# Optimization experiments

Hardware: AMD Instinct MI355X
Metric: run time of the kernel (lower is better)

## Reference

```python
import jax, jax.numpy as jnp
import numpy as np

D_MODEL = 256
N_HEADS = 8
HEAD_DIM = D_MODEL // N_HEADS


def setup_inputs() -> dict:
    key = jax.random.key(0)
    ks = jax.random.split(key, 10)
    B, L, D = 2, 2048, D_MODEL
    s = 1.0 / np.sqrt(D)
    inp = {
        "x": jax.random.normal(ks[0], (B, L, D), dtype=jnp.float32),
        "Wq": jax.random.normal(ks[1], (D, D), dtype=jnp.float32) * s,
        "bq": jnp.zeros((D,), jnp.float32),
        "Wk": jax.random.normal(ks[2], (D, D), dtype=jnp.float32) * s,
        "bk": jnp.zeros((D,), jnp.float32),
        "Wv": jax.random.normal(ks[3], (D, D), dtype=jnp.float32) * s,
        "bv": jnp.zeros((D,), jnp.float32),
        "u": jax.random.normal(ks[4], (N_HEADS, 1, 1), dtype=jnp.float32) * 0.1,
        "Wo": jax.random.normal(ks[5], (D, D), dtype=jnp.float32) * s,
        "bo": jnp.zeros((D,), jnp.float32),
    }
    return inp


def reference(x, Wq, bq, Wk, bk, Wv, bv, u, Wo, bo):
    B, L, D = x.shape
    H, hd = N_HEADS, HEAD_DIM

    def proj(W, b):  # torch Linear: x @ W.T + b -> [B,H,L,hd]
        return (x @ W.T + b).reshape(B, L, H, hd).transpose(0, 2, 1, 3)

    Q, K, V = proj(Wq, bq), proj(Wk, bk), proj(Wv, bv)

    scores = jnp.einsum("bhqd,bhkd->bhqk", Q, K) / np.sqrt(hd)
    attn_series = jax.nn.softmax(scores, axis=-1)  # [B,H,L,L]

    pos = jnp.arange(L, dtype=jnp.float32)
    dist = jnp.abs(pos[None, :] - pos[:, None])  # [L,L]
    # prior per head: exp(-d^2 / (2*(u^2+1e-6))), normalized over last dim
    prior = jnp.exp(-(dist[None] ** 2) / (2.0 * (u ** 2 + 1e-6)))  # [H,L,L]
    prior = prior / (prior.sum(axis=-1, keepdims=True) + 1e-6)

    discrepancy = jnp.abs(attn_series - prior[None]).mean(axis=(1, 2))  # [B,L]

    out = jnp.einsum("bhqk,bhkd->bhqd", attn_series, V)
    out = out.transpose(0, 2, 1, 3).reshape(B, L, D)
    out = out @ Wo.T + bo
    return out, discrepancy
```

## Files before the change

### kernel.cpp

```cpp
#include <hip/hip_runtime.h>
#include <hip/hip_bf16.h>
#include <math.h>

#define LSEQ 2048
#define DMODEL 256
#define NH 8
#define HD 32

typedef __attribute__((ext_vector_type(8))) short bf16x8;
typedef __attribute__((ext_vector_type(4))) float f32x4;

#define MFMA __builtin_amdgcn_mfma_f32_16x16x32_bf16

__device__ __forceinline__ short f2bf(float x) {
  __hip_bfloat16 h = __float2bfloat16(x);
  return __builtin_bit_cast(short, h);
}
__device__ __forceinline__ float bf2f(short s) {
  __hip_bfloat16 h = __builtin_bit_cast(__hip_bfloat16, s);
  return __bfloat162float(h);
}
__device__ __forceinline__ short bftrunc(float x) {
  return (short)(__builtin_bit_cast(unsigned int, x) >> 16);
}
__device__ __forceinline__ float fexp2(float x) {
#if __has_builtin(__builtin_amdgcn_exp2f)
  return __builtin_amdgcn_exp2f(x);
#else
  return __expf(x * 0.6931471805599453f);
#endif
}
__device__ __forceinline__ float flog2(float x) {
#if __has_builtin(__builtin_amdgcn_logf)
  return __builtin_amdgcn_logf(x);
#else
  return __logf(x) * 1.4426950408889634f;
#endif
}

__global__ __launch_bounds__(256) void aux_kernel(
    const float* __restrict__ Wq, const float* __restrict__ Wk,
    const float* __restrict__ Wv, const float* __restrict__ Wo,
    const float* __restrict__ u,
    short* __restrict__ Wh,
    short* __restrict__ Woh, short* __restrict__ Wol,
    float* __restrict__ Eb, float* __restrict__ Zb,
    float* __restrict__ disc)
{
  __shared__ float Cs[LSEQ];
  __shared__ float part[256];
  const int tid = threadIdx.x;
  if (blockIdx.x < 256) {
    const int i4 = (blockIdx.x * 256 + tid) * 4;
    if (i4 < 196608) {
      int row = i4 >> 8, col = i4 & 255;
      const float* W = (row < 256) ? Wq : (row < 512) ? Wk : Wv;
      float4 v = *(const float4*)(W + (row & 255) * 256 + col);
      *(short4*)(Wh + i4) = make_short4(f2bf(v.x), f2bf(v.y), f2bf(v.z), f2bf(v.w));
    } else {
      int j = i4 - 196608;
      float4 v = *(const float4*)(Wo + j);
      short h0 = f2bf(v.x), h1 = f2bf(v.y), h2 = f2bf(v.z), h3 = f2bf(v.w);
      *(short4*)(Woh + j) = make_short4(h0, h1, h2, h3);
      *(short4*)(Wol + j) = make_short4(bftrunc(v.x - bf2f(h0)), bftrunc(v.y - bf2f(h1)),
                                        bftrunc(v.z - bf2f(h2)), bftrunc(v.w - bf2f(h3)));
    }
    return;
  }
  const int h = blockIdx.x - 256;
  const float uu = u[h];
  const float den = 2.0f * (uu * uu + 1e-6f);
  float e[8]; float run = 0.f;
  const int base = tid * 8;
#pragma unroll
  for (int j = 0; j < 8; ++j) {
    float d = (float)(base + j);
    e[j] = __expf(-(d * d) / den);
    run += e[j];
  }
  part[tid] = run;
  __syncthreads();
  for (int off = 1; off < 256; off <<= 1) {
    float v = (tid >= off) ? part[tid - off] : 0.f;
    __syncthreads();
    part[tid] += v;
    __syncthreads();
  }
  float c = part[tid] - run;
#pragma unroll
  for (int j = 0; j < 8; ++j) {
    c += e[j];
    Cs[base + j] = c;
    Eb[h * LSEQ + base + j] = e[j];
  }
  __syncthreads();
  const float E0 = Cs[0];
  for (int i = tid; i < LSEQ; i += 256) {
    float s = Cs[i] + Cs[LSEQ - 1 - i] - E0;
    Zb[h * LSEQ + i] = 1.0f / (s + 1e-6f);
  }
  for (int i = tid; i < 512; i += 256) disc[h * 512 + i] = 0.f;
}

__global__ __launch_bounds__(256) void qkv_gemm(
    const float* __restrict__ x,
    const short* __restrict__ Bh,
    const float* __restrict__ bq, const float* __restrict__ bk,
    const float* __restrict__ bv,
    short* __restrict__ Qf, short* __restrict__ Kf, short* __restrict__ Vf)
{
  const int tid = threadIdx.x, w = tid >> 6, lane = tid & 63;
  const int l15 = lane & 15, q4 = lane >> 4;
  const int m0 = blockIdx.x * 64, n0 = blockIdx.y * 64;
  const int mrow = m0 + w * 16 + l15;
  f32x4 acc[4] = {{0,0,0,0},{0,0,0,0},{0,0,0,0},{0,0,0,0}};
  for (int k0 = 0; k0 < 256; k0 += 32) {
    const float* xp = &x[(size_t)mrow * 256 + k0 + q4 * 8];
    float4 a = *(const float4*)xp;
    float4 c = *(const float4*)(xp + 4);
    bf16x8 ah;
    ah[0] = f2bf(a.x); ah[1] = f2bf(a.y); ah[2] = f2bf(a.z); ah[3] = f2bf(a.w);
    ah[4] = f2bf(c.x); ah[5] = f2bf(c.y); ah[6] = f2bf(c.z); ah[7] = f2bf(c.w);
#pragma unroll
    for (int nt = 0; nt < 4; ++nt) {
      const size_t bi = (size_t)(n0 + nt * 16 + l15) * 256 + k0 + q4 * 8;
      bf16x8 bh = *(const bf16x8*)&Bh[bi];
      acc[nt] = MFMA(ah, bh, acc[nt], 0, 0, 0);
    }
  }
  const int type = n0 >> 8;
  const int n0l = n0 & 255;
  const float* bias = (type == 0) ? bq : (type == 1) ? bk : bv;
  const float qls = 0.25503489f;
#pragma unroll
  for (int nt = 0; nt < 4; ++nt) {
    const int col = n0l + nt * 16 + l15;
    const float bvv = bias[col];
    const int hh = col >> 5, dloc = col & 31;
#pragma unroll
    for (int r = 0; r < 4; ++r) {
      const int m = m0 + w * 16 + q4 * 4 + r;
      float v = acc[nt][r] + bvv;
      const int bb = m >> 11, mm = m & 2047, rr = mm & 15;
      if (type == 2) {
        const int kt128 = mm >> 7, low7 = mm & 127;
        const int wv = (low7 >> 4) & 3, ph = low7 >> 6;
        const int c = ph * 16 + rr;
        const size_t idx =
          ((((((size_t)bb * 8 + hh) * 16 + kt128) * 4 + wv) * 2 + (dloc >> 4)) * 64
           + (c >> 3) * 16 + (dloc & 15)) * 8 + (c & 7);
        Vf[idx] = f2bf(v);
      } else if (type == 0) {
        const int qblk = mm >> 5, rg = (mm >> 4) & 1;
        const size_t idx =
          (((((size_t)bb * 8 + hh) * 64 + qblk) * 2 + rg) * 64
           + (dloc >> 3) * 16 + rr) * 8 + (dloc & 7);
        Qf[idx] = f2bf(v * qls);
      } else {
        const int g = mm >> 4;
        const size_t idx =
          ((((size_t)bb * 8 + hh) * 128 + g) * 64
           + (dloc >> 3) * 16 + rr) * 8 + (dloc & 7);
        Kf[idx] = f2bf(v);
      }
    }
  }
}

__global__ __launch_bounds__(256) void out_gemm(
    const short* __restrict__ Ah, const short* __restrict__ Al,
    const short* __restrict__ Bh, const short* __restrict__ Bl,
    const float* __restrict__ bias, float* __restrict__ C)
{
  const int tid = threadIdx.x, w = tid >> 6, lane = tid & 63;
  const int l15 = lane & 15, q4 = lane >> 4;
  const int m0 = blockIdx.x * 64, n0 = blockIdx.y * 64;
  const int mrow = m0 + w * 16 + l15;
  f32x4 acc[4] = {{0,0,0,0},{0,0,0,0},{0,0,0,0},{0,0,0,0}};
  for (int k0 = 0; k0 < 256; k0 += 32) {
    bf16x8 ah = *(const bf16x8*)&Ah[(size_t)mrow * 256 + k0 + q4 * 8];
    bf16x8 al = *(const bf16x8*)&Al[(size_t)mrow * 256 + k0 + q4 * 8];
#pragma unroll
    for (int nt = 0; nt < 4; ++nt) {
      const size_t bi = (size_t)(n0 + nt * 16 + l15) * 256 + k0 + q4 * 8;
      bf16x8 bh = *(const bf16x8*)&Bh[bi];
      bf16x8 bl = *(const bf16x8*)&Bl[bi];
      acc[nt] = MFMA(ah, bh, acc[nt], 0, 0, 0);
      acc[nt] = MFMA(al, bh, acc[nt], 0, 0, 0);
      acc[nt] = MFMA(ah, bl, acc[nt], 0, 0, 0);
    }
  }
#pragma unroll
  for (int nt = 0; nt < 4; ++nt) {
    const int col = n0 + nt * 16 + l15;
    const float bvv = bias[col];
#pragma unroll
    for (int r = 0; r < 4; ++r) {
      const int m = m0 + w * 16 + q4 * 4 + r;
      C[(size_t)m * 256 + col] = acc[nt][r] + bvv;
    }
  }
}

__global__ __launch_bounds__(256, 4) void attn_kernel(
    const short* __restrict__ Qf, const short* __restrict__ Kf,
    const short* __restrict__ Vf,
    const float* __restrict__ Eb, const float* __restrict__ Zb,
    short* __restrict__ Ohb, short* __restrict__ Olb,
    float* __restrict__ disc)
{
  __shared__ short Pt[4][32][40];
  __shared__ float Elds[192];
  __shared__ float dcol[LSEQ];
  __shared__ float lpart[4][32];
  __shared__ float izlds[32];

  const int tid = threadIdx.x, w = tid >> 6, lane = tid & 63;
  const int l15 = lane & 15, q4 = lane >> 4;
  const int flat = blockIdx.x + 64 * (blockIdx.y + 8 * blockIdx.z);
  const int slot = flat >> 3;
  const int g = (flat & 7) | ((slot >> 6) << 3);
  const int h = g & 7, b = g >> 3;
  const int q0 = (slot & 63) * 32;
  const int bh = b * NH + h;

  for (int i = tid; i < LSEQ; i += 256) dcol[i] = 0.f;
  if (tid < 192) Elds[tid] = Eb[h * LSEQ + tid];
  if (tid < 32)  izlds[tid] = Zb[h * LSEQ + q0 + tid];

  const bf16x8* Qf8 = (const bf16x8*)Qf;
  const bf16x8* Kf8 = (const bf16x8*)Kf;
  const bf16x8* Vf8 = (const bf16x8*)Vf;

  bf16x8 qh[2];
#pragma unroll
  for (int rg = 0; rg < 2; ++rg)
    qh[rg] = Qf8[((((size_t)bh * 64 + (q0 >> 5)) * 2 + rg)) * 64 + lane];
  __syncthreads();

  const size_t kfb = (size_t)bh * 128;
  const size_t vfb = (size_t)bh * 16;

  float lac[2][4] = {{0,0,0,0},{0,0,0,0}};
#pragma unroll 2
  for (int kt = 0; kt < LSEQ; kt += 128) {
    bf16x8 k0 = Kf8[(kfb + (kt >> 4) + w) * 64 + lane];
    bf16x8 k1 = Kf8[(kfb + (kt >> 4) + 4 + w) * 64 + lane];
#pragma unroll
    for (int rg = 0; rg < 2; ++rg) {
      f32x4 s0 = {0.f, 0.f, 0.f, 0.f};
      s0 = MFMA(qh[rg], k0, s0, 0, 0, 0);
      f32x4 s1 = {0.f, 0.f, 0.f, 0.f};
      s1 = MFMA(qh[rg], k1, s1, 0, 0, 0);
#pragma unroll
      for (int r = 0; r < 4; ++r) lac[rg][r] += fexp2(s0[r]) + fexp2(s1[r]);
    }
  }
#pragma unroll
  for (int rg = 0; rg < 2; ++rg)
#pragma unroll
    for (int r = 0; r < 4; ++r) {
      float v = lac[rg][r];
      v += __shfl_xor(v, 1); v += __shfl_xor(v, 2);
      v += __shfl_xor(v, 4); v += __shfl_xor(v, 8);
      lac[rg][r] = v;
    }
  if (l15 == 0) {
#pragma unroll
    for (int rg = 0; rg < 2; ++rg)
#pragma unroll
      for (int r = 0; r < 4; ++r) lpart[w][rg * 16 + q4 * 4 + r] = lac[rg][r];
  }
  __syncthreads();
  f32x4 sinit[2];
#pragma unroll
  for (int rg = 0; rg < 2; ++rg)
#pragma unroll
    for (int r = 0; r < 4; ++r) {
      const int qi = rg * 16 + q4 * 4 + r;
      sinit[rg][r] = -flog2(lpart[0][qi] + lpart[1][qi] + lpart[2][qi] + lpart[3][qi]);
    }

  f32x4 oacc[2][2] = {{{0,0,0,0},{0,0,0,0}},{{0,0,0,0},{0,0,0,0}}};
#pragma unroll 2
  for (int kt = 0; kt < LSEQ; kt += 128) {
    bf16x8 kh0 = Kf8[(kfb + (kt >> 4) + w) * 64 + lane];
    bf16x8 kh1 = Kf8[(kfb + (kt >> 4) + 4 + w) * 64 + lane];
    bf16x8 vb0 = Vf8[(((vfb + (kt >> 7)) * 4 + w) * 2 + 0) * 64 + lane];
    bf16x8 vb1 = Vf8[(((vfb + (kt >> 7)) * 4 + w) * 2 + 1) * 64 + lane];
#pragma unroll
    for (int ph = 0; ph < 2; ++ph) {
      bf16x8 kbh = ph ? kh1 : kh0;
      const int c0 = kt + ph * 64 + w * 16;
      const int kg = c0 + l15;
      const int dd = c0 - q0;
      const bool near = (dd >= -96) && (dd <= 96);
      float dsum = 0.f;
#pragma unroll
      for (int rg = 0; rg < 2; ++rg) {
        f32x4 s = sinit[rg];
        s = MFMA(qh[rg], kbh, s, 0, 0, 0);
#pragma unroll
        for (int r = 0; r < 4; ++r) {
          float p = fexp2(s[r]);
          Pt[w][rg * 16 + q4 * 4 + r][ph * 16 + l15] = bftrunc(p);
          if (near) {
            int qrow = q0 + rg * 16 + q4 * 4 + r;
            int dist = (qrow >= kg) ? (qrow - kg) : (kg - qrow);
            dsum += fabsf(p - Elds[dist] * izlds[rg * 16 + q4 * 4 + r]);
          } else {
            dsum += p;
          }
        }
      }
      dsum += __shfl_xor(dsum, 16);
      dsum += __shfl_xor(dsum, 32);
      if (q4 == 0) atomicAdd(&dcol[kg], dsum);
    }
#pragma unroll
    for (int rg = 0; rg < 2; ++rg) {
      bf16x8 pa = *(const bf16x8*)&Pt[w][rg * 16 + l15][q4 * 8];
      oacc[rg][0] = MFMA(pa, vb0, oacc[rg][0], 0, 0, 0);
      oacc[rg][1] = MFMA(pa, vb1, oacc[rg][1], 0, 0, 0);
    }
  }

  __syncthreads();
  float* Ored = (float*)&Pt[0][0][0];
#pragma unroll
  for (int dt = 0; dt < 2; ++dt) {
#pragma unroll
    for (int rg = 0; rg < 2; ++rg)
#pragma unroll
      for (int r = 0; r < 4; ++r)
        Ored[(w * 32 + rg * 16 + q4 * 4 + r) * 17 + l15] = oacc[rg][dt][r];
    __syncthreads();
    for (int t = tid; t < 512; t += 256) {
      const int q = t >> 4, d = t & 15;
      float v = Ored[(q) * 17 + d] + Ored[(32 + q) * 17 + d] +
                Ored[(64 + q) * 17 + d] + Ored[(96 + q) * 17 + d];
      const size_t oo = ((size_t)b * LSEQ + q0 + q) * DMODEL + h * HD + dt * 16 + d;
      short hi = f2bf(v);
      Ohb[oo] = hi;
      Olb[oo] = bftrunc(v - bf2f(hi));
    }
    __syncthreads();
  }
  const float sc = 1.0f / (float)(NH * LSEQ);
  for (int i = tid; i < LSEQ; i += 256)
    atomicAdd(&disc[(size_t)b * LSEQ + i], dcol[i] * sc);
}

extern "C" void kernel_launch(void* const* d_in, const int* in_sizes, int n_in,
                              void* d_out, int out_size, void* d_ws, size_t ws_size,
                              hipStream_t stream)
{
  const float* x  = (const float*)d_in[0];
  const float* Wq = (const float*)d_in[1];
  const float* bq = (const float*)d_in[2];
  const float* Wk = (const float*)d_in[3];
  const float* bk = (const float*)d_in[4];
  const float* Wv = (const float*)d_in[5];
  const float* bv = (const float*)d_in[6];
  const float* u  = (const float*)d_in[7];
  const float* Wo = (const float*)d_in[8];
  const float* bo = (const float*)d_in[9];

  float* out  = (float*)d_out;
  float* disc = out + (size_t)2 * LSEQ * DMODEL;

  char* w8 = (char*)d_ws;
  const size_t MB = 1u << 20;
  short* Qfb = (short*)(w8);
  short* Kfb = (short*)(w8 + 2 * MB);
  short* Vfb = (short*)(w8 + 4 * MB);
  short* Ohb = (short*)(w8 + 6 * MB);
  short* Olb = (short*)(w8 + 8 * MB);
  short* Wh  = (short*)(w8 + 10 * MB);
  short* Woh = (short*)(w8 + 10 * MB + 393216);
  short* Wol = (short*)(w8 + 10 * MB + 524288);
  float* Eb  = (float*)(w8 + 11 * MB);
  float* Zb  = (float*)(w8 + 11 * MB + 65536);

  aux_kernel<<<264, 256, 0, stream>>>(Wq, Wk, Wv, Wo, u, Wh, Woh, Wol,
                                      Eb, Zb, disc);
  qkv_gemm<<<dim3(64, 12), 256, 0, stream>>>(x, Wh, bq, bk, bv,
                                             Qfb, Kfb, Vfb);
  attn_kernel<<<dim3(LSEQ / 32, NH, 2), 256, 0, stream>>>(Qfb, Kfb, Vfb,
                                                          Eb, Zb, Ohb, Olb, disc);
  out_gemm<<<dim3(64, 4), 256, 0, stream>>>(Ohb, Olb, Woh, Wol, bo, out);
}
```

Baseline: 158.0 us.

## Halve attention query tile and replace discrepancy atomics with partial buffer reduction

The attention kernel now processes 16 query rows per block instead of 32, doubling the grid to 2048 blocks and raising launch-bound occupancy to 8 blocks per CU. The per-block shared dcol array and global atomicAdd of discrepancy column sums are removed. Each block instead writes bf16 partial column sums to a workspace buffer, and a new disc_reduce kernel sums them deterministically. This adds a 16 MB-scale partial buffer write/read and an extra launch, and it re-reads K/V twice as often across blocks. Storing the partials in bf16 also loses some precision in the discrepancy output.

```diff
diff --git a/kernel.cpp b/kernel.cpp
--- a/kernel.cpp
+++ b/kernel.cpp
@@ -44,8 +44,7 @@
     const float* __restrict__ u,
     short* __restrict__ Wh,
     short* __restrict__ Woh, short* __restrict__ Wol,
-    float* __restrict__ Eb, float* __restrict__ Zb,
-    float* __restrict__ disc)
+    float* __restrict__ Eb, float* __restrict__ Zb)
 {
   __shared__ float Cs[LSEQ];
   __shared__ float part[256];
@@ -99,7 +98,6 @@
     float s = Cs[i] + Cs[LSEQ - 1 - i] - E0;
     Zb[h * LSEQ + i] = 1.0f / (s + 1e-6f);
   }
-  for (int i = tid; i < 512; i += 256) disc[h * 512 + i] = 0.f;
 }
 
 __global__ __launch_bounds__(256) void qkv_gemm(
@@ -202,86 +200,73 @@
   }
 }
 
-__global__ __launch_bounds__(256, 4) void attn_kernel(
+__global__ __launch_bounds__(256, 8) void attn_kernel(
     const short* __restrict__ Qf, const short* __restrict__ Kf,
     const short* __restrict__ Vf,
     const float* __restrict__ Eb, const float* __restrict__ Zb,
     short* __restrict__ Ohb, short* __restrict__ Olb,
-    float* __restrict__ disc)
-{
-  __shared__ short Pt[4][32][40];
+    short* __restrict__ Dp)
+{
+  __shared__ short Pt[4][16][40];
   __shared__ float Elds[192];
-  __shared__ float dcol[LSEQ];
-  __shared__ float lpart[4][32];
-  __shared__ float izlds[32];
+  __shared__ float lpart[4][16];
+  __shared__ float izlds[16];
 
   const int tid = threadIdx.x, w = tid >> 6, lane = tid & 63;
   const int l15 = lane & 15, q4 = lane >> 4;
-  const int flat = blockIdx.x + 64 * (blockIdx.y + 8 * blockIdx.z);
+  const int flat = blockIdx.x + 128 * (blockIdx.y + 8 * blockIdx.z);
   const int slot = flat >> 3;
-  const int g = (flat & 7) | ((slot >> 6) << 3);
+  const int g = (flat & 7) | ((slot >> 7) << 3);
   const int h = g & 7, b = g >> 3;
-  const int q0 = (slot & 63) * 32;
+  const int qslot = slot & 127, q0 = qslot * 16;
   const int bh = b * NH + h;
 
-  for (int i = tid; i < LSEQ; i += 256) dcol[i] = 0.f;
   if (tid < 192) Elds[tid] = Eb[h * LSEQ + tid];
-  if (tid < 32)  izlds[tid] = Zb[h * LSEQ + q0 + tid];
+  if (tid < 16)  izlds[tid] = Zb[h * LSEQ + q0 + tid];
 
   const bf16x8* Qf8 = (const bf16x8*)Qf;
   const bf16x8* Kf8 = (const bf16x8*)Kf;
   const bf16x8* Vf8 = (const bf16x8*)Vf;
 
-  bf16x8 qh[2];
-#pragma unroll
-  for (int rg = 0; rg < 2; ++rg)
-    qh[rg] = Qf8[((((size_t)bh * 64 + (q0 >> 5)) * 2 + rg)) * 64 + lane];
+  bf16x8 qh = Qf8[((size_t)bh * 128 + qslot) * 64 + lane];
   __syncthreads();
 
   const size_t kfb = (size_t)bh * 128;
   const size_t vfb = (size_t)bh * 16;
 
-  float lac[2][4] = {{0,0,0,0},{0,0,0,0}};
+  float lac[4] = {0.f, 0.f, 0.f, 0.f};
 #pragma unroll 2
   for (int kt = 0; kt < LSEQ; kt += 128) {
     bf16x8 k0 = Kf8[(kfb + (kt >> 4) + w) * 64 + lane];
     bf16x8 k1 = Kf8[(kfb + (kt >> 4) + 4 + w) * 64 + lane];
-#pragma unroll
-    for (int rg = 0; rg < 2; ++rg) {
-      f32x4 s0 = {0.f, 0.f, 0.f, 0.f};
-      s0 = MFMA(qh[rg], k0, s0, 0, 0, 0);
-      f32x4 s1 = {0.f, 0.f, 0.f, 0.f};
-      s1 = MFMA(qh[rg], k1, s1, 0, 0, 0);
-#pragma unroll
-      for (int r = 0; r < 4; ++r) lac[rg][r] += fexp2(s0[r]) + fexp2(s1[r]);
-    }
-  }
-#pragma unroll
-  for (int rg = 0; rg < 2; ++rg)
-#pragma unroll
-    for (int r = 0; r < 4; ++r) {
-      float v = lac[rg][r];
-      v += __shfl_xor(v, 1); v += __shfl_xor(v, 2);
-      v += __shfl_xor(v, 4); v += __shfl_xor(v, 8);
-      lac[rg][r] = v;
-    }
+    f32x4 s0 = {0.f, 0.f, 0.f, 0.f};
+    s0 = MFMA(qh, k0, s0, 0, 0, 0);
+    f32x4 s1 = {0.f, 0.f, 0.f, 0.f};
+    s1 = MFMA(qh, k1, s1, 0, 0, 0);
+#pragma unroll
+    for (int r = 0; r < 4; ++r) lac[r] += fexp2(s0[r]) + fexp2(s1[r]);
+  }
+#pragma unroll
+  for (int r = 0; r < 4; ++r) {
+    float v = lac[r];
+    v += __shfl_xor(v, 1); v += __shfl_xor(v, 2);
+    v += __shfl_xor(v, 4); v += __shfl_xor(v, 8);
+    lac[r] = v;
+  }
   if (l15 == 0) {
 #pragma unroll
-    for (int rg = 0; rg < 2; ++rg)
-#pragma unroll
-      for (int r = 0; r < 4; ++r) lpart[w][rg * 16 + q4 * 4 + r] = lac[rg][r];
-  }
-  __syncthreads();
-  f32x4 sinit[2];
-#pragma unroll
-  for (int rg = 0; rg < 2; ++rg)
-#pragma unroll
-    for (int r = 0; r < 4; ++r) {
-      const int qi = rg * 16 + q4 * 4 + r;
-      sinit[rg][r] = -flog2(lpart[0][qi] + lpart[1][qi] + lpart[2][qi] + lpart[3][qi]);
-    }
-
-  f32x4 oacc[2][2] = {{{0,0,0,0},{0,0,0,0}},{{0,0,0,0},{0,0,0,0}}};
+    for (int r = 0; r < 4; ++r) lpart[w][q4 * 4 + r] = lac[r];
+  }
+  __syncthreads();
+  f32x4 sinit;
+#pragma unroll
+  for (int r = 0; r < 4; ++r) {
+    const int qi = q4 * 4 + r;
+    sinit[r] = -flog2(lpart[0][qi] + lpart[1][qi] + lpart[2][qi] + lpart[3][qi]);
+  }
+
+  const size_t drow = (size_t)(g * 128 + qslot) * LSEQ;
+  f32x4 oacc[2] = {{0,0,0,0},{0,0,0,0}};
 #pragma unroll 2
   for (int kt = 0; kt < LSEQ; kt += 128) {
     bf16x8 kh0 = Kf8[(kfb + (kt >> 4) + w) * 64 + lane];
@@ -296,33 +281,27 @@
       const int dd = c0 - q0;
       const bool near = (dd >= -96) && (dd <= 96);
       float dsum = 0.f;
-#pragma unroll
-      for (int rg = 0; rg < 2; ++rg) {
-        f32x4 s = sinit[rg];
-        s = MFMA(qh[rg], kbh, s, 0, 0, 0);
-#pragma unroll
-        for (int r = 0; r < 4; ++r) {
-          float p = fexp2(s[r]);
-          Pt[w][rg * 16 + q4 * 4 + r][ph * 16 + l15] = bftrunc(p);
-          if (near) {
-            int qrow = q0 + rg * 16 + q4 * 4 + r;
-            int dist = (qrow >= kg) ? (qrow - kg) : (kg - qrow);
-            dsum += fabsf(p - Elds[dist] * izlds[rg * 16 + q4 * 4 + r]);
-          } else {
-            dsum += p;
-          }
+      f32x4 s = sinit;
+      s = MFMA(qh, kbh, s, 0, 0, 0);
+#pragma unroll
+      for (int r = 0; r < 4; ++r) {
+        float p = fexp2(s[r]);
+        Pt[w][q4 * 4 + r][ph * 16 + l15] = bftrunc(p);
+        if (near) {
+          int qrow = q0 + q4 * 4 + r;
+          int dist = (qrow >= kg) ? (qrow - kg) : (kg - qrow);
+          dsum += fabsf(p - Elds[dist] * izlds[q4 * 4 + r]);
+        } else {
+          dsum += p;
         }
       }
       dsum += __shfl_xor(dsum, 16);
       dsum += __shfl_xor(dsum, 32);
-      if (q4 == 0) atomicAdd(&dcol[kg], dsum);
-    }
-#pragma unroll
-    for (int rg = 0; rg < 2; ++rg) {
-      bf16x8 pa = *(const bf16x8*)&Pt[w][rg * 16 + l15][q4 * 8];
-      oacc[rg][0] = MFMA(pa, vb0, oacc[rg][0], 0, 0, 0);
-      oacc[rg][1] = MFMA(pa, vb1, oacc[rg][1], 0, 0, 0);
-    }
+      if (q4 == 0) Dp[drow + kg] = f2bf(dsum);
+    }
+    bf16x8 pa = *(const bf16x8*)&Pt[w][l15][q4 * 8];
+    oacc[0] = MFMA(pa, vb0, oacc[0], 0, 0, 0);
+    oacc[1] = MFMA(pa, vb1, oacc[1], 0, 0, 0);
   }
 
   __syncthreads();
@@ -330,15 +309,13 @@
 #pragma unroll
   for (int dt = 0; dt < 2; ++dt) {
 #pragma unroll
-    for (int rg = 0; rg < 2; ++rg)
-#pragma unroll
-      for (int r = 0; r < 4; ++r)
-        Ored[(w * 32 + rg * 16 + q4 * 4 + r) * 17 + l15] = oacc[rg][dt][r];
+    for (int r = 0; r < 4; ++r)
+      Ored[(w * 16 + q4 * 4 + r) * 17 + l15] = oacc[dt][r];
     __syncthreads();
-    for (int t = tid; t < 512; t += 256) {
-      const int q = t >> 4, d = t & 15;
-      float v = Ored[(q) * 17 + d] + Ored[(32 + q) * 17 + d] +
-                Ored[(64 + q) * 17 + d] + Ored[(96 + q) * 17 + d];
+    {
+      const int q = tid >> 4, d = tid & 15;
+      float v = Ored[q * 17 + d] + Ored[(16 + q) * 17 + d] +
+                Ored[(32 + q) * 17 + d] + Ored[(48 + q) * 17 + d];
       const size_t oo = ((size_t)b * LSEQ + q0 + q) * DMODEL + h * HD + dt * 16 + d;
       short hi = f2bf(v);
       Ohb[oo] = hi;
@@ -346,9 +323,28 @@
     }
     __syncthreads();
   }
-  const float sc = 1.0f / (float)(NH * LSEQ);
-  for (int i = tid; i < LSEQ; i += 256)
-    atomicAdd(&disc[(size_t)b * LSEQ + i], dcol[i] * sc);
+}
+
+__global__ __launch_bounds__(256) void disc_reduce(
+    const short* __restrict__ Dp, float* __restrict__ disc)
+{
+  __shared__ float red[8][33];
+  const int tid = threadIdx.x;
+  const int b = blockIdx.x >> 6;
+  const int kb = (blockIdx.x & 63) * 32;
+  const int k = kb + (tid & 31), sg = tid >> 5;
+  float acc = 0.f;
+  const short* base = Dp + ((size_t)b * 1024 + (size_t)sg * 128) * LSEQ + k;
+#pragma unroll 4
+  for (int i = 0; i < 128; ++i) acc += bf2f(base[(size_t)i * LSEQ]);
+  red[sg][tid & 31] = acc;
+  __syncthreads();
+  if (tid < 32) {
+    float v = 0.f;
+#pragma unroll
+    for (int s2 = 0; s2 < 8; ++s2) v += red[s2][tid];
+    disc[b * LSEQ + kb + tid] = v * (1.0f / ((float)NH * (float)LSEQ));
+  }
 }
 
 extern "C" void kernel_launch(void* const* d_in, const int* in_sizes, int n_in,
@@ -381,12 +377,12 @@
   short* Wol = (short*)(w8 + 10 * MB + 524288);
   float* Eb  = (float*)(w8 + 11 * MB);
   float* Zb  = (float*)(w8 + 11 * MB + 65536);
-
-  aux_kernel<<<264, 256, 0, stream>>>(Wq, Wk, Wv, Wo, u, Wh, Woh, Wol,
-                                      Eb, Zb, disc);
-  qkv_gemm<<<dim3(64, 12), 256, 0, stream>>>(x, Wh, bq, bk, bv,
-                                             Qfb, Kfb, Vfb);
-  attn_kernel<<<dim3(LSEQ / 32, NH, 2), 256, 0, stream>>>(Qfb, Kfb, Vfb,
-                                                          Eb, Zb, Ohb, Olb, disc);
+  short* Dp  = (short*)(w8 + 12 * MB);
+
+  aux_kernel<<<264, 256, 0, stream>>>(Wq, Wk, Wv, Wo, u, Wh, Woh, Wol, Eb, Zb);
+  qkv_gemm<<<dim3(64, 12), 256, 0, stream>>>(x, Wh, bq, bk, bv, Qfb, Kfb, Vfb);
+  attn_kernel<<<dim3(128, 8, 2), 256, 0, stream>>>(Qfb, Kfb, Vfb, Eb, Zb,
+                                                   Ohb, Olb, Dp);
+  disc_reduce<<<128, 256, 0, stream>>>(Dp, disc);
   out_gemm<<<dim3(64, 4), 256, 0, stream>>>(Ohb, Olb, Woh, Wol, bo, out);
 }
```

Result: no change. 156.7 us (-0.8%).
